# Optimization experiments

Hardware: AMD Instinct MI355X
Metric: run time of the kernel (lower is better)

## Reference

```python
import jax, jax.numpy as jnp
import numpy as np

EPS = 1e-6  # torch F.cosine_similarity eps


def setup_inputs() -> dict:
    key = jax.random.key(0)
    k1, = jax.random.split(key, 1)
    N, M, D = 1024, 10, 768
    dvecs = jax.random.normal(k1, (N, M, D), dtype=jnp.float32)
    w = jnp.full((1,), 10.0, dtype=jnp.float32)   # init_w
    b = jnp.full((1,), -5.0, dtype=jnp.float32)   # init_b
    return {"dvecs": dvecs, "w": w, "b": b}


def _ge2e_softmax_loss(dvecs, w, b):
    N, M, D = dvecs.shape
    sums = jnp.sum(dvecs, axis=1)                      # (N, D)
    ctrds = sums / M                                   # full centroids
    excl = (sums[:, None, :] - dvecs) / (M - 1)        # (N, M, D) leave-one-out centroids

    dnorm = jnp.maximum(jnp.linalg.norm(dvecs, axis=-1), EPS)   # (N, M)
    cnorm = jnp.maximum(jnp.linalg.norm(ctrds, axis=-1), EPS)   # (N,)
    enorm = jnp.maximum(jnp.linalg.norm(excl, axis=-1), EPS)    # (N, M)

    # cosine sim of every utterance to every full centroid: (N, M, N)
    sim_all = jnp.einsum('nmd,kd->nmk', dvecs, ctrds) / (dnorm[:, :, None] * cnorm[None, None, :])
    # cosine sim of each utterance to its own excluded centroid: (N, M)
    sim_own = jnp.sum(dvecs * excl, axis=-1) / (dnorm * enorm)

    own_mask = jnp.eye(N, dtype=bool)[:, None, :]      # (N, 1, N)
    sim = jnp.where(own_mask, sim_own[:, :, None], sim_all)

    sim = sim * w[0] + b[0]
    losses = -jax.nn.log_softmax(sim, axis=2)          # (N, M, N)
    # pick entry [s, u, s] for each utterance
    own = jnp.take_along_axis(losses, jnp.broadcast_to(jnp.arange(N)[:, None, None], (N, M, 1)), axis=2)
    return jnp.sum(own)


def reference(dvecs, w, b):
    return _ge2e_softmax_loss(dvecs, w, b)
```

## Files before the change

kernel.cpp:

```cpp
#include <hip/hip_runtime.h>
#include <hip/hip_bf16.h>

#define EPS 1e-6f

typedef __attribute__((ext_vector_type(4))) float f32x4;

__device__ inline unsigned int pack_fp8x4(float x, float y, float z, float w) {
  int r = 0;
  r = __builtin_amdgcn_cvt_pk_fp8_f32(x, y, r, false);
  r = __builtin_amdgcn_cvt_pk_fp8_f32(z, w, r, true);
  return (unsigned int)r;
}

__global__ void __launch_bounds__(192) ge2e_pre(
    const float* __restrict__ dv, unsigned int* __restrict__ a8u,
    unsigned int* __restrict__ c8u, float* __restrict__ simown,
    float* __restrict__ rowsum, float* __restrict__ out) {
  const int n = blockIdx.x, t = threadIdx.x;
  if (n == 0 && t == 0) out[0] = 0.f;
  const float* base = dv + (size_t)n * 7680;
  float4 v[10];
  float4 s4 = make_float4(0.f, 0.f, 0.f, 0.f);
#pragma unroll
  for (int m = 0; m < 10; ++m) {
    v[m] = *reinterpret_cast<const float4*>(&base[m * 768 + 4 * t]);
    s4.x += v[m].x; s4.y += v[m].y; s4.z += v[m].z; s4.w += v[m].w;
  }
  float part[21];
#pragma unroll
  for (int m = 0; m < 10; ++m) {
    part[m]      = v[m].x * s4.x + v[m].y * s4.y + v[m].z * s4.z + v[m].w * s4.w;
    part[10 + m] = v[m].x * v[m].x + v[m].y * v[m].y + v[m].z * v[m].z + v[m].w * v[m].w;
  }
  part[20] = s4.x * s4.x + s4.y * s4.y + s4.z * s4.z + s4.w * s4.w;
#pragma unroll
  for (int k = 0; k < 21; ++k) {
#pragma unroll
    for (int off = 32; off >= 1; off >>= 1) part[k] += __shfl_xor(part[k], off);
  }
  __shared__ float red[3][21];
  __shared__ float bc[21];
  const int lane = t & 63, wid = t >> 6;
  if (lane == 0) {
#pragma unroll
    for (int k = 0; k < 21; ++k) red[wid][k] = part[k];
  }
  __syncthreads();
  if (t < 21) bc[t] = red[0][t] + red[1][t] + red[2][t];
  __syncthreads();
  const float ss = bc[20];
  const float rc = 1.0f / fmaxf(sqrtf(ss), 10.0f * EPS);
  c8u[n * 192 + t] = pack_fp8x4(s4.x * rc, s4.y * rc, s4.z * rc, s4.w * rc);
#pragma unroll
  for (int m = 0; m < 10; ++m) {
    float rd = 1.0f / fmaxf(sqrtf(bc[10 + m]), EPS);
    a8u[(size_t)(n * 10 + m) * 192 + t] =
        pack_fp8x4(v[m].x * rd, v[m].y * rd, v[m].z * rd, v[m].w * rd);
  }
  if (t < 10) {
    float dot = bc[t], sq = bc[10 + t];
    float dn = fmaxf(sqrtf(sq), EPS);
    float en = fmaxf(sqrtf(fmaxf(ss - 2.f * dot + sq, 0.f)) * (1.0f / 9.0f), EPS);
    simown[n * 10 + t] = ((dot - sq) * (1.0f / 9.0f)) / (dn * en);
    rowsum[n * 10 + t] = 0.f;
  }
}

__global__ void __launch_bounds__(256, 5) ge2e_gemm(
    const unsigned char* __restrict__ a8, const unsigned char* __restrict__ c8,
    const float* __restrict__ simown, const float* __restrict__ wp,
    float* __restrict__ rowsum) {
  __shared__ unsigned char As[2][2][64 * 32];
  __shared__ unsigned char Bs[2][2][128 * 32];
  const int t = threadIdx.x;
  const int lane = t & 63, wid = t >> 6;
  const int bx = blockIdx.x;
  const int wg = (bx & 7) * 160 + (bx >> 3);
  const int rb = wg >> 3, cb = wg & 7;
  const int row0 = rb * 64, col0 = cb * 128;
  const int wr = wid >> 1, wc = wid & 1;
  const int l15 = lane & 15, lg = lane >> 4;

  f32x4 acc[2][4];
#pragma unroll
  for (int i = 0; i < 2; ++i)
#pragma unroll
    for (int j = 0; j < 4; ++j) acc[i][j] = (f32x4){0.f, 0.f, 0.f, 0.f};

  auto STAGE = [&](int buf, int kk) {
#pragma unroll
    for (int jj = 0; jj < 3; ++jj) {
      const int s = wid * 3 + jj;
      if (s < 4) {
        const int c = s * 64 + lane;
        const int half = c >> 7, row = (c >> 1) & 63, k16 = c & 1;
        const unsigned char* src =
            a8 + (size_t)(row0 + row) * 768 + kk + half * 32 + k16 * 16;
        unsigned char* dst = &As[buf][0][0] + s * 1024;
        __builtin_amdgcn_global_load_lds(
            (const __attribute__((address_space(1))) unsigned int*)src,
            (__attribute__((address_space(3))) unsigned int*)dst, 16, 0, 0);
      } else {
        const int c = (s - 4) * 64 + lane;
        const int half = c >> 8, row = (c >> 1) & 127, k16 = c & 1;
        const unsigned char* src =
            c8 + (size_t)(col0 + row) * 768 + kk + half * 32 + k16 * 16;
        unsigned char* dst = &Bs[buf][0][0] + (s - 4) * 1024;
        __builtin_amdgcn_global_load_lds(
            (const __attribute__((address_space(1))) unsigned int*)src,
            (__attribute__((address_space(3))) unsigned int*)dst, 16, 0, 0);
      }
    }
  };
  auto COMPUTE = [&](int buf) {
    long long af[2][2], bq[4][2];
#pragma unroll
    for (int i = 0; i < 2; ++i)
#pragma unroll
      for (int h = 0; h < 2; ++h)
        af[i][h] = *(const long long*)&As[buf][h][(wr * 32 + i * 16 + l15) * 32 + lg * 8];
#pragma unroll
    for (int j = 0; j < 4; ++j)
#pragma unroll
      for (int h = 0; h < 2; ++h)
        bq[j][h] = *(const long long*)&Bs[buf][h][(wc * 64 + j * 16 + l15) * 32 + lg * 8];
#pragma unroll
    for (int h = 0; h < 2; ++h)
#pragma unroll
      for (int i = 0; i < 2; ++i)
#pragma unroll
        for (int j = 0; j < 4; ++j)
          acc[i][j] = __builtin_amdgcn_mfma_f32_16x16x32_fp8_fp8(
              af[i][h], bq[j][h], acc[i][j], 0, 0, 0);
  };

  STAGE(0, 0);
  asm volatile("s_waitcnt vmcnt(0)" ::: "memory");
  __builtin_amdgcn_s_barrier();
  int cur = 0;
  for (int tt = 0; tt < 11; ++tt) {
    STAGE(cur ^ 1, (tt + 1) * 64);
    COMPUTE(cur);
    asm volatile("s_waitcnt vmcnt(0)" ::: "memory");
    __builtin_amdgcn_s_barrier();
    cur ^= 1;
  }
  COMPUTE(cur);

  const float wv = wp[0];
  const int R0 = row0 + wr * 32, C0 = col0 + wc * 64;
#pragma unroll
  for (int i = 0; i < 2; ++i) {
#pragma unroll
    for (int r = 0; r < 4; ++r) {
      const int grow = R0 + i * 16 + lg * 4 + r;
      const int ownc = grow / 10;
      float sm = 0.f;
#pragma unroll
      for (int j = 0; j < 4; ++j) {
        const int gcol = C0 + j * 16 + l15;
        float vv = wv * acc[i][j][r];
        if (gcol == ownc) vv = wv * simown[grow];
        sm += __expf(vv);
      }
#pragma unroll
      for (int off = 1; off < 16; off <<= 1) sm += __shfl_xor(sm, off, 16);
      if (l15 == 0) atomicAdd(&rowsum[grow], sm);
    }
  }
}

__global__ void __launch_bounds__(256) ge2e_final(
    const float* __restrict__ rowsum, const float* __restrict__ simown,
    const float* __restrict__ wp, float* __restrict__ out) {
  const int i = blockIdx.x * 256 + threadIdx.x;
  const float wv = wp[0];
  float loss = logf(rowsum[i]) - wv * simown[i];
#pragma unroll
  for (int off = 32; off >= 1; off >>= 1) loss += __shfl_xor(loss, off);
  __shared__ float red[4];
  const int lane = threadIdx.x & 63, wid = threadIdx.x >> 6;
  if (lane == 0) red[wid] = loss;
  __syncthreads();
  if (threadIdx.x == 0) atomicAdd(out, red[0] + red[1] + red[2] + red[3]);
}

extern "C" void kernel_launch(void* const* d_in, const int* in_sizes, int n_in,
                              void* d_out, int out_size, void* d_ws, size_t ws_size,
                              hipStream_t stream) {
  (void)in_sizes; (void)n_in; (void)out_size; (void)ws_size;
  const float* dv = (const float*)d_in[0];
  const float* wp = (const float*)d_in[1];

  unsigned char* a8 = (unsigned char*)d_ws;
  unsigned char* c8 = (unsigned char*)d_ws + 7864320;
  float* simown = (float*)((char*)d_ws + 8650752);
  float* rowsum = (float*)((char*)d_ws + 8691712);
  float* out = (float*)d_out;

  ge2e_pre<<<1024, 192, 0, stream>>>(dv, (unsigned int*)a8, (unsigned int*)c8,
                                     simown, rowsum, out);
  ge2e_gemm<<<1280, 256, 0, stream>>>(a8, c8, simown, wp, rowsum);
  ge2e_final<<<40, 256, 0, stream>>>(rowsum, simown, wp, out);
}
```

Before: 47.02 us.

## Enlarge GEMM tiles to 320x128 with 8 waves and XOR-swizzled LDS

Rebuilds the FP8 MFMA GEMM to use 320x128 output tiles per 512-thread block, 256 blocks in total, and a K-step of 128 bytes, so each staged operand is reused across more MFMAs. The LDS layout is XOR-swizzled by row to avoid bank conflicts, and the pipeline waits only on the previous stage with vmcnt(7) before the barrier. It also raises MFMA priority with setprio. In exchange, 256 blocks on a 256-CU device gives only one wave of blocks per CU, and the larger accumulator raises register pressure.

```diff
diff --git a/kernel.cpp b/kernel.cpp
--- a/kernel.cpp
+++ b/kernel.cpp
@@ -66,100 +66,114 @@
   }
 }
 
-__global__ void __launch_bounds__(256, 5) ge2e_gemm(
+__global__ void __launch_bounds__(512, 2) ge2e_gemm(
     const unsigned char* __restrict__ a8, const unsigned char* __restrict__ c8,
     const float* __restrict__ simown, const float* __restrict__ wp,
     float* __restrict__ rowsum) {
-  __shared__ unsigned char As[2][2][64 * 32];
-  __shared__ unsigned char Bs[2][2][128 * 32];
+  __shared__ __align__(16) unsigned char As[2][40960];
+  __shared__ __align__(16) unsigned char Bs[2][16384];
   const int t = threadIdx.x;
   const int lane = t & 63, wid = t >> 6;
   const int bx = blockIdx.x;
-  const int wg = (bx & 7) * 160 + (bx >> 3);
+  const int wg = (bx & 7) * 32 + (bx >> 3);
   const int rb = wg >> 3, cb = wg & 7;
-  const int row0 = rb * 64, col0 = cb * 128;
-  const int wr = wid >> 1, wc = wid & 1;
+  const int row0 = rb * 320, col0 = cb * 128;
+  const int wm = wid >> 1, wn = wid & 1;
   const int l15 = lane & 15, lg = lane >> 4;
-
-  f32x4 acc[2][4];
-#pragma unroll
-  for (int i = 0; i < 2; ++i)
+  const int l8 = lane >> 3, sl = lane & 7;
+  const int sk16 = sl ^ l8;
+
+  f32x4 acc[5][4];
+#pragma unroll
+  for (int i = 0; i < 5; ++i)
 #pragma unroll
     for (int j = 0; j < 4; ++j) acc[i][j] = (f32x4){0.f, 0.f, 0.f, 0.f};
 
-  auto STAGE = [&](int buf, int kk) {
-#pragma unroll
-    for (int jj = 0; jj < 3; ++jj) {
-      const int s = wid * 3 + jj;
-      if (s < 4) {
-        const int c = s * 64 + lane;
-        const int half = c >> 7, row = (c >> 1) & 63, k16 = c & 1;
+  auto STAGE = [&](int buf, int ks) {
+#pragma unroll
+    for (int j = 0; j < 7; ++j) {
+      const int g = wid * 7 + j;
+      if (g < 40) {
         const unsigned char* src =
-            a8 + (size_t)(row0 + row) * 768 + kk + half * 32 + k16 * 16;
-        unsigned char* dst = &As[buf][0][0] + s * 1024;
+            a8 + (size_t)(row0 + g * 8 + l8) * 768 + ks * 128 + sk16 * 16;
         __builtin_amdgcn_global_load_lds(
             (const __attribute__((address_space(1))) unsigned int*)src,
-            (__attribute__((address_space(3))) unsigned int*)dst, 16, 0, 0);
+            (__attribute__((address_space(3))) unsigned int*)&As[buf][g * 1024],
+            16, 0, 0);
       } else {
-        const int c = (s - 4) * 64 + lane;
-        const int half = c >> 8, row = (c >> 1) & 127, k16 = c & 1;
         const unsigned char* src =
-            c8 + (size_t)(col0 + row) * 768 + kk + half * 32 + k16 * 16;
-        unsigned char* dst = &Bs[buf][0][0] + (s - 4) * 1024;
+            c8 + (size_t)(col0 + (g - 40) * 8 + l8) * 768 + ks * 128 + sk16 * 16;
         __builtin_amdgcn_global_load_lds(
             (const __attribute__((address_space(1))) unsigned int*)src,
-            (__attribute__((address_space(3))) unsigned int*)dst, 16, 0, 0);
+            (__attribute__((address_space(3))) unsigned int*)&Bs[buf][(g - 40) * 1024],
+            16, 0, 0);
       }
     }
   };
+
+  auto ldA = [&](int buf, int kt, int kh, int fr) -> long long {
+    const int row = wm * 80 + fr * 16 + l15;
+    const int k16 = (kt * 4 + kh * 2 + (lg >> 1)) ^ (row & 7);
+    return *(const long long*)&As[buf][row * 128 + k16 * 16 + (lg & 1) * 8];
+  };
+  auto ldB = [&](int buf, int kt, int kh, int fc) -> long long {
+    const int row = wn * 64 + fc * 16 + l15;
+    const int k16 = (kt * 4 + kh * 2 + (lg >> 1)) ^ (row & 7);
+    return *(const long long*)&Bs[buf][row * 128 + k16 * 16 + (lg & 1) * 8];
+  };
+
   auto COMPUTE = [&](int buf) {
-    long long af[2][2], bq[4][2];
-#pragma unroll
-    for (int i = 0; i < 2; ++i)
-#pragma unroll
-      for (int h = 0; h < 2; ++h)
-        af[i][h] = *(const long long*)&As[buf][h][(wr * 32 + i * 16 + l15) * 32 + lg * 8];
-#pragma unroll
-    for (int j = 0; j < 4; ++j)
-#pragma unroll
-      for (int h = 0; h < 2; ++h)
-        bq[j][h] = *(const long long*)&Bs[buf][h][(wc * 64 + j * 16 + l15) * 32 + lg * 8];
-#pragma unroll
-    for (int h = 0; h < 2; ++h)
-#pragma unroll
-      for (int i = 0; i < 2; ++i)
-#pragma unroll
-        for (int j = 0; j < 4; ++j)
-          acc[i][j] = __builtin_amdgcn_mfma_f32_16x16x32_fp8_fp8(
-              af[i][h], bq[j][h], acc[i][j], 0, 0, 0);
+#pragma unroll
+    for (int kt = 0; kt < 2; ++kt) {
+      long long af[5][2], bf[4][2];
+#pragma unroll
+      for (int fc = 0; fc < 4; ++fc)
+#pragma unroll
+        for (int kh = 0; kh < 2; ++kh) bf[fc][kh] = ldB(buf, kt, kh, fc);
+#pragma unroll
+      for (int fr = 0; fr < 5; ++fr)
+#pragma unroll
+        for (int kh = 0; kh < 2; ++kh) af[fr][kh] = ldA(buf, kt, kh, fr);
+      __builtin_amdgcn_s_setprio(1);
+#pragma unroll
+      for (int kh = 0; kh < 2; ++kh)
+#pragma unroll
+        for (int fr = 0; fr < 5; ++fr)
+#pragma unroll
+          for (int fc = 0; fc < 4; ++fc)
+            acc[fr][fc] = __builtin_amdgcn_mfma_f32_16x16x32_fp8_fp8(
+                af[fr][kh], bf[fc][kh], acc[fr][fc], 0, 0, 0);
+      __builtin_amdgcn_s_setprio(0);
+    }
   };
 
   STAGE(0, 0);
-  asm volatile("s_waitcnt vmcnt(0)" ::: "memory");
-  __builtin_amdgcn_s_barrier();
-  int cur = 0;
-  for (int tt = 0; tt < 11; ++tt) {
-    STAGE(cur ^ 1, (tt + 1) * 64);
-    COMPUTE(cur);
-    asm volatile("s_waitcnt vmcnt(0)" ::: "memory");
+#pragma unroll
+  for (int s = 0; s < 6; ++s) {
+    if (s < 5) {
+      STAGE((s + 1) & 1, s + 1);
+      asm volatile("s_waitcnt vmcnt(7)" ::: "memory");
+    } else {
+      asm volatile("s_waitcnt vmcnt(0)" ::: "memory");
+    }
     __builtin_amdgcn_s_barrier();
-    cur ^= 1;
-  }
-  COMPUTE(cur);
+    COMPUTE(s & 1);
+    if (s < 5) __builtin_amdgcn_s_barrier();
+  }
 
   const float wv = wp[0];
-  const int R0 = row0 + wr * 32, C0 = col0 + wc * 64;
-#pragma unroll
-  for (int i = 0; i < 2; ++i) {
+  const int R0 = row0 + wm * 80, C0 = col0 + wn * 64;
+#pragma unroll
+  for (int fr = 0; fr < 5; ++fr) {
 #pragma unroll
     for (int r = 0; r < 4; ++r) {
-      const int grow = R0 + i * 16 + lg * 4 + r;
+      const int grow = R0 + fr * 16 + lg * 4 + r;
       const int ownc = grow / 10;
       float sm = 0.f;
 #pragma unroll
-      for (int j = 0; j < 4; ++j) {
-        const int gcol = C0 + j * 16 + l15;
-        float vv = wv * acc[i][j][r];
+      for (int fc = 0; fc < 4; ++fc) {
+        const int gcol = C0 + fc * 16 + l15;
+        float vv = wv * acc[fr][fc][r];
         if (gcol == ownc) vv = wv * simown[grow];
         sm += __expf(vv);
       }
@@ -200,6 +214,6 @@
 
   ge2e_pre<<<1024, 192, 0, stream>>>(dv, (unsigned int*)a8, (unsigned int*)c8,
                                      simown, rowsum, out);
-  ge2e_gemm<<<1280, 256, 0, stream>>>(a8, c8, simown, wp, rowsum);
+  ge2e_gemm<<<256, 512, 0, stream>>>(a8, c8, simown, wp, rowsum);
   ge2e_final<<<40, 256, 0, stream>>>(rowsum, simown, wp, out);
 }
```

Result: faster. 43.96 us (-6.5%).
